# Kernel optimization log

Hardware: AMD Instinct MI355X
Metric: run time of the kernel (lower is better)

## Reference

```python
import jax, jax.numpy as jnp
import numpy as np


def setup_inputs() -> dict:
    key = jax.random.key(0)
    rain_hr = jax.random.normal(key, (16, 8, 1, 512, 512), dtype=jnp.float32)
    return {"rain_hr": rain_hr}


def reference(rain_hr):
    B, T, C, H, W = rain_hr.shape
    rain_mean = rain_hr.mean(axis=1)              # [B, C, H, W]

    fft = jnp.fft.fft2(rain_mean)                 # complex [B, C, H, W]
    power = jnp.abs(fft) ** 2                     # [B, C, H, W]

    # Integer radius map (torch: sqrt(...).long() truncates toward zero)
    ch, cw = H // 2, W // 2
    y = jnp.arange(H, dtype=jnp.float32) - ch
    x = jnp.arange(W, dtype=jnp.float32) - cw
    radius = jnp.sqrt(x[None, :] ** 2 + y[:, None] ** 2).astype(jnp.int32)  # [H, W]

    max_radius = min(H, W) // 2

    # power[..., mask].mean() == sum over (B, C, pixels at radius r) / (B*C*count_r)
    power_hw = power.sum(axis=(0, 1))             # [H, W]
    flat_r = radius.ravel()
    # out-of-range radii (>= max_radius) are dropped by segment_sum
    seg_sum = jax.ops.segment_sum(power_hw.ravel(), flat_r, num_segments=max_radius)
    counts = jax.ops.segment_sum(jnp.ones((H * W,), jnp.float32), flat_r, num_segments=max_radius)

    cnt = counts[1:]                               # radii 1 .. max_radius-1
    denom = jnp.maximum(cnt, 1.0) * (B * C)
    gen_spectrum = jnp.where(cnt > 0, seg_sum[1:] / denom, 0.0)

    k = jnp.arange(1, max_radius, dtype=jnp.float32)
    ref = k ** (-5.0 / 3.0)
    ref = ref / (ref.sum() + 1e-8)

    gen_norm = gen_spectrum / (gen_spectrum.sum() + 1e-8)
    loss = jnp.mean((gen_norm - ref) ** 2)
    return loss
```

## Files before the change

### kernel.cpp

```cpp
#include <hip/hip_runtime.h>
#include <math.h>

#define N 512
#define PLANE ((size_t)N * N)
#define NEG2PI (-6.28318530717958647692f)

__device__ inline void dft8(float (&xr)[8], float (&xi)[8]) {
    const float S = 0.70710678118654752440f;
    float t0r = xr[0] + xr[4], t0i = xi[0] + xi[4];
    float t4r = xr[0] - xr[4], t4i = xi[0] - xi[4];
    float t1r = xr[1] + xr[5], t1i = xi[1] + xi[5];
    float t5r = xr[1] - xr[5], t5i = xi[1] - xi[5];
    float t2r = xr[2] + xr[6], t2i = xi[2] + xi[6];
    float t6r = xr[2] - xr[6], t6i = xi[2] - xi[6];
    float t3r = xr[3] + xr[7], t3i = xi[3] + xi[7];
    float t7r = xr[3] - xr[7], t7i = xi[3] - xi[7];
    float o1r = S * (t5r + t5i), o1i = S * (t5i - t5r);
    float o2r = t6i,             o2i = -t6r;
    float o3r = S * (t7i - t7r), o3i = -S * (t7r + t7i);
    float p0r = t0r + t2r, p0i = t0i + t2i;
    float p1r = t1r + t3r, p1i = t1i + t3i;
    float q0r = t0r - t2r, q0i = t0i - t2i;
    float q1r = t1i - t3i, q1i = -(t1r - t3r);
    xr[0] = p0r + p1r; xi[0] = p0i + p1i;
    xr[4] = p0r - p1r; xi[4] = p0i - p1i;
    xr[2] = q0r + q1r; xi[2] = q0i + q1i;
    xr[6] = q0r - q1r; xi[6] = q0i - q1i;
    float r0r = t4r + o2r, r0i = t4i + o2i;
    float r1r = o1r + o3r, r1i = o1i + o3i;
    float u0r = t4r - o2r, u0i = t4i - o2i;
    float u1r = o1i - o3i, u1i = -(o1r - o3r);
    xr[1] = r0r + r1r; xi[1] = r0i + r1i;
    xr[5] = r0r - r1r; xi[5] = r0i - r1i;
    xr[3] = u0r + u1r; xi[3] = u0i + u1i;
    xr[7] = u0r - u1r; xi[7] = u0i - u1i;
}

__device__ inline void twiddle_apply(float (&xr)[8], float (&xi)[8], float ang1) {
    float ts, tc;
    __sincosf(ang1, &ts, &tc);
    float wr = tc, wi = ts;
    #pragma unroll
    for (int k = 1; k < 8; ++k) {
        float nr = xr[k] * wr - xi[k] * wi;
        float ni = xr[k] * wi + xi[k] * wr;
        xr[k] = nr; xi[k] = ni;
        float w2r = wr * tc - wi * ts;
        float w2i = wr * ts + wi * tc;
        wr = w2r; wi = w2i;
    }
}

__device__ inline void fft512_wave(float (&xr)[8], float (&xi)[8],
                                   float* sre, float* sim, const int l) {
    dft8(xr, xi);
    twiddle_apply(xr, xi, (NEG2PI / 512.0f) * (float)l);
    const int w0 = l + (l >> 3);
    #pragma unroll
    for (int k = 0; k < 8; ++k) { sre[72 * k + w0] = xr[k]; sim[72 * k + w0] = xi[k]; }
    const int i2 = l & 7;
    const int rbase = 72 * (l >> 3) + i2;
    #pragma unroll
    for (int q = 0; q < 8; ++q) { xr[q] = sre[rbase + 9 * q]; xi[q] = sim[rbase + 9 * q]; }
    dft8(xr, xi);
    twiddle_apply(xr, xi, (NEG2PI / 64.0f) * (float)i2);
    #pragma unroll
    for (int k = 0; k < 8; ++k) { sre[rbase + 9 * k] = xr[k]; sim[rbase + 9 * k] = xi[k]; }
    const int r3 = 9 * l;
    #pragma unroll
    for (int q = 0; q < 8; ++q) { xr[q] = sre[r3 + q]; xi[q] = sim[r3 + q]; }
    dft8(xr, xi);
}

__global__ __launch_bounds__(256, 4) void kern_rowfft(const float* __restrict__ in,
                                                      float2* __restrict__ ws) {
    __shared__ float sRe[4][576];
    __shared__ float sIm[4][576];
    const int wv = threadIdx.x >> 6;
    const int l  = threadIdx.x & 63;
    const int y  = blockIdx.x * 4 + wv;
    const int j  = blockIdx.y;
    const float* baseA = in + ((size_t)j * 8) * PLANE + (size_t)y * N;
    const float* baseB = in + ((size_t)(j + 8) * 8) * PLANE + (size_t)y * N;
    float* re = sRe[wv];
    float* im = sIm[wv];
    #pragma unroll
    for (int c0 = 0; c0 < 2; ++c0) {
        const int c = l + 64 * c0;
        float4 sa = make_float4(0.f, 0.f, 0.f, 0.f);
        float4 sb = make_float4(0.f, 0.f, 0.f, 0.f);
        #pragma unroll
        for (int tt = 0; tt < 8; ++tt) {
            float4 a = *(const float4*)(baseA + tt * PLANE + 4 * c);
            float4 b = *(const float4*)(baseB + tt * PLANE + 4 * c);
            sa.x += a.x; sa.y += a.y; sa.z += a.z; sa.w += a.w;
            sb.x += b.x; sb.y += b.y; sb.z += b.z; sb.w += b.w;
        }
        const int i0 = 4 * c;
        const int p0 = i0 + (i0 >> 3);
        re[p0 + 0] = sa.x * 0.125f; re[p0 + 1] = sa.y * 0.125f;
        re[p0 + 2] = sa.z * 0.125f; re[p0 + 3] = sa.w * 0.125f;
        im[p0 + 0] = sb.x * 0.125f; im[p0 + 1] = sb.y * 0.125f;
        im[p0 + 2] = sb.z * 0.125f; im[p0 + 3] = sb.w * 0.125f;
    }
    float xr[8], xi[8];
    #pragma unroll
    for (int q = 0; q < 8; ++q) {
        const int p = l + (l >> 3) + 72 * q;
        xr[q] = re[p]; xi[q] = im[p];
    }
    fft512_wave(xr, xi, re, im, l);
    float2* wp = ws + ((size_t)j << 18) + ((size_t)y << 9);
    #pragma unroll
    for (int k = 0; k < 8; ++k) {
        wp[64 * k + 8 * (l & 7) + (l >> 3)] = make_float2(xr[k], xi[k]);
    }
}

__global__ __launch_bounds__(512, 4) void kern_colfft(const float2* __restrict__ ws,
                                                      float* __restrict__ gseg,
                                                      float* __restrict__ gcnt) {
    __shared__ float sA[8 * 576];
    __shared__ float sB[8 * 576];
    __shared__ float lseg[256];
    __shared__ float lcnt[256];
    const int w   = threadIdx.x >> 6;
    const int l   = threadIdx.x & 63;
    const int fx0 = blockIdx.x * 8;
    const int j   = blockIdx.y;
    if (threadIdx.x < 256) { lseg[threadIdx.x] = 0.f; lcnt[threadIdx.x] = 0.f; }
    const float2* base = ws + ((size_t)j << 18) + fx0;
    #pragma unroll
    for (int i = 0; i < 8; ++i) {
        const int y = (w << 6) + (i << 3) + (l >> 3);
        const int f = l & 7;
        float2 v = base[((size_t)y << 9) + f];
        sA[y * 9 + f] = v.x;
        sB[y * 9 + f] = v.y;
    }
    __syncthreads();
    float xr[8], xi[8];
    #pragma unroll
    for (int q = 0; q < 8; ++q) {
        const int y = l + (q << 6);
        xr[q] = sA[y * 9 + w];
        xi[q] = sB[y * 9 + w];
    }
    __syncthreads();
    fft512_wave(xr, xi, sA + w * 576, sB + w * 576, l);
    const int dx  = fx0 + w - 256;
    const int dx2 = dx * dx;
    #pragma unroll
    for (int k = 0; k < 8; ++k) {
        const int fy = 64 * k + 8 * (l & 7) + (l >> 3);
        const int dy = fy - 256;
        const int d2 = dx2 + dy * dy;
        int r = (int)sqrtf((float)d2);
        if ((r + 1) * (r + 1) <= d2) r++;
        else if (r * r > d2) r--;
        if (r >= 1 && r < 256) {
            atomicAdd(&lseg[r], xr[k] * xr[k] + xi[k] * xi[k]);
            if (j == 0) atomicAdd(&lcnt[r], 1.0f);
        }
    }
    __syncthreads();
    const int t = threadIdx.x;
    if (t < 256) {
        if (lseg[t] != 0.f) atomicAdd(&gseg[j * 256 + t], lseg[t]);
    } else if (j == 0) {
        if (lcnt[t - 256] != 0.f) atomicAdd(&gcnt[t - 256], lcnt[t - 256]);
    }
}

__global__ __launch_bounds__(256) void kern_loss(const float* __restrict__ gseg,
                                                 const float* __restrict__ gcnt,
                                                 float* __restrict__ out) {
    __shared__ float red[256];
    const int t = threadIdx.x;
    float gen = 0.f, refv = 0.f;
    if (t >= 1) {
        float s = 0.f;
        #pragma unroll
        for (int j = 0; j < 8; ++j) s += gseg[j * 256 + t];
        float c = gcnt[t];
        gen  = (c > 0.f) ? s / (fmaxf(c, 1.f) * 16.0f) : 0.f;
        refv = powf((float)t, -5.0f / 3.0f);
    }
    red[t] = gen; __syncthreads();
    for (int off = 128; off > 0; off >>= 1) {
        if (t < off) red[t] += red[t + off];
        __syncthreads();
    }
    const float sgen = red[0]; __syncthreads();
    red[t] = refv; __syncthreads();
    for (int off = 128; off > 0; off >>= 1) {
        if (t < off) red[t] += red[t + off];
        __syncthreads();
    }
    const float sref = red[0]; __syncthreads();
    const float gn = gen  / (sgen + 1e-8f);
    const float rn = refv / (sref + 1e-8f);
    red[t] = (gn - rn) * (gn - rn); __syncthreads();
    for (int off = 128; off > 0; off >>= 1) {
        if (t < off) red[t] += red[t + off];
        __syncthreads();
    }
    if (t == 0) out[0] = red[0] / 255.0f;
}

extern "C" void kernel_launch(void* const* d_in, const int* in_sizes, int n_in,
                              void* d_out, int out_size, void* d_ws, size_t ws_size,
                              hipStream_t stream) {
    const float* in = (const float*)d_in[0];
    float2* planes = (float2*)d_ws;
    float* bins = (float*)((char*)d_ws + (size_t)8 * N * N * sizeof(float2));
    float* gseg = bins;
    float* gcnt = bins + 8 * 256;
    hipMemsetAsync(bins, 0, (8 * 256 + 256) * sizeof(float), stream);
    kern_rowfft<<<dim3(128, 8), 256, 0, stream>>>(in, planes);
    kern_colfft<<<dim3(64, 8), 512, 0, stream>>>(planes, gseg, gcnt);
    kern_loss<<<1, 256, 0, stream>>>(gseg, gcnt, (float*)d_out);
}
```

Before: 216.8 us.

## Fold memset and loss kernel into FFT kernels; shrink column-FFT blocks

Zeroing of the bins moves from a hipMemsetAsync into the row-FFT kernel, and the separate loss kernel is replaced by a last-block-done pattern inside the column FFT, using an atomic counter. The column FFT now runs four columns per 256-thread block, giving twice as many blocks, and loads them with float4 reads. This removes two launches and their gaps and raises block-level parallelism. In exchange it adds an atomic counter plus fences, and correctness now depends on the counter reset in the row kernel finishing before the column kernel starts.

Measured after the change: 252.0 us. 1.16x slower.

```diff
diff --git a/kernel.cpp b/kernel.cpp
--- a/kernel.cpp
+++ b/kernel.cpp
@@ -4,6 +4,7 @@
 #define N 512
 #define PLANE ((size_t)N * N)
 #define NEG2PI (-6.28318530717958647692f)
+#define NBLK_COL 1024
 
 __device__ inline void dft8(float (&xr)[8], float (&xi)[8]) {
     const float S = 0.70710678118654752440f;
@@ -73,13 +74,20 @@
 }
 
 __global__ __launch_bounds__(256, 4) void kern_rowfft(const float* __restrict__ in,
-                                                      float2* __restrict__ ws) {
+                                                      float2* __restrict__ ws,
+                                                      float* __restrict__ bins,
+                                                      unsigned int* __restrict__ done) {
     __shared__ float sRe[4][576];
     __shared__ float sIm[4][576];
     const int wv = threadIdx.x >> 6;
     const int l  = threadIdx.x & 63;
     const int y  = blockIdx.x * 4 + wv;
     const int j  = blockIdx.y;
+    if (blockIdx.x == 0 && j == 0) {
+        for (int i = threadIdx.x; i < 8 * 256 + 256; i += 256) bins[i] = 0.f;
+        if (threadIdx.x == 0)
+            __hip_atomic_store(done, 0u, __ATOMIC_RELAXED, __HIP_MEMORY_SCOPE_AGENT);
+    }
     const float* baseA = in + ((size_t)j * 8) * PLANE + (size_t)y * N;
     const float* baseB = in + ((size_t)(j + 8) * 8) * PLANE + (size_t)y * N;
     float* re = sRe[wv];
@@ -117,34 +125,40 @@
     }
 }
 
-__global__ __launch_bounds__(512, 4) void kern_colfft(const float2* __restrict__ ws,
+__global__ __launch_bounds__(256, 4) void kern_colfft(const float2* __restrict__ ws,
                                                       float* __restrict__ gseg,
-                                                      float* __restrict__ gcnt) {
-    __shared__ float sA[8 * 576];
-    __shared__ float sB[8 * 576];
+                                                      float* __restrict__ gcnt,
+                                                      unsigned int* __restrict__ done,
+                                                      float* __restrict__ out) {
+    __shared__ float sA[2560];
+    __shared__ float sB[2560];
     __shared__ float lseg[256];
     __shared__ float lcnt[256];
-    const int w   = threadIdx.x >> 6;
-    const int l   = threadIdx.x & 63;
-    const int fx0 = blockIdx.x * 8;
+    __shared__ int isLast;
+    const int t   = threadIdx.x;
+    const int w   = t >> 6;
+    const int l   = t & 63;
+    const int fx0 = blockIdx.x * 4;
     const int j   = blockIdx.y;
-    if (threadIdx.x < 256) { lseg[threadIdx.x] = 0.f; lcnt[threadIdx.x] = 0.f; }
+    lseg[t] = 0.f;
+    lcnt[t] = 0.f;
     const float2* base = ws + ((size_t)j << 18) + fx0;
     #pragma unroll
-    for (int i = 0; i < 8; ++i) {
-        const int y = (w << 6) + (i << 3) + (l >> 3);
-        const int f = l & 7;
-        float2 v = base[((size_t)y << 9) + f];
-        sA[y * 9 + f] = v.x;
-        sB[y * 9 + f] = v.y;
+    for (int i = 0; i < 4; ++i) {
+        const int g  = i * 256 + t;
+        const int y  = g >> 1;
+        const int fp = g & 1;
+        float4 v = *(const float4*)(base + ((size_t)y << 9) + 2 * fp);
+        sA[y * 5 + 2 * fp + 0] = v.x;  sB[y * 5 + 2 * fp + 0] = v.y;
+        sA[y * 5 + 2 * fp + 1] = v.z;  sB[y * 5 + 2 * fp + 1] = v.w;
     }
     __syncthreads();
     float xr[8], xi[8];
     #pragma unroll
     for (int q = 0; q < 8; ++q) {
         const int y = l + (q << 6);
-        xr[q] = sA[y * 9 + w];
-        xi[q] = sB[y * 9 + w];
+        xr[q] = sA[y * 5 + w];
+        xi[q] = sB[y * 5 + w];
     }
     __syncthreads();
     fft512_wave(xr, xi, sA + w * 576, sB + w * 576, l);
@@ -164,48 +178,50 @@
         }
     }
     __syncthreads();
-    const int t = threadIdx.x;
-    if (t < 256) {
-        if (lseg[t] != 0.f) atomicAdd(&gseg[j * 256 + t], lseg[t]);
-    } else if (j == 0) {
-        if (lcnt[t - 256] != 0.f) atomicAdd(&gcnt[t - 256], lcnt[t - 256]);
-    }
-}
-
-__global__ __launch_bounds__(256) void kern_loss(const float* __restrict__ gseg,
-                                                 const float* __restrict__ gcnt,
-                                                 float* __restrict__ out) {
-    __shared__ float red[256];
-    const int t = threadIdx.x;
+    if (lseg[t] != 0.f) atomicAdd(&gseg[j * 256 + t], lseg[t]);
+    if (j == 0 && lcnt[t] != 0.f) atomicAdd(&gcnt[t], lcnt[t]);
+    __syncthreads();
+    if (t == 0) {
+        __threadfence();
+        unsigned int old = __hip_atomic_fetch_add(done, 1u, __ATOMIC_ACQ_REL,
+                                                  __HIP_MEMORY_SCOPE_AGENT);
+        isLast = (old == NBLK_COL - 1) ? 1 : 0;
+    }
+    __syncthreads();
+    if (!isLast) return;
+    __threadfence();
     float gen = 0.f, refv = 0.f;
     if (t >= 1) {
         float s = 0.f;
         #pragma unroll
-        for (int j = 0; j < 8; ++j) s += gseg[j * 256 + t];
-        float c = gcnt[t];
+        for (int jj = 0; jj < 8; ++jj)
+            s += __hip_atomic_load(&gseg[jj * 256 + t], __ATOMIC_RELAXED,
+                                   __HIP_MEMORY_SCOPE_AGENT);
+        float c = __hip_atomic_load(&gcnt[t], __ATOMIC_RELAXED,
+                                    __HIP_MEMORY_SCOPE_AGENT);
         gen  = (c > 0.f) ? s / (fmaxf(c, 1.f) * 16.0f) : 0.f;
         refv = powf((float)t, -5.0f / 3.0f);
     }
-    red[t] = gen; __syncthreads();
+    lseg[t] = gen; __syncthreads();
     for (int off = 128; off > 0; off >>= 1) {
-        if (t < off) red[t] += red[t + off];
+        if (t < off) lseg[t] += lseg[t + off];
         __syncthreads();
     }
-    const float sgen = red[0]; __syncthreads();
-    red[t] = refv; __syncthreads();
+    const float sgen = lseg[0]; __syncthreads();
+    lseg[t] = refv; __syncthreads();
     for (int off = 128; off > 0; off >>= 1) {
-        if (t < off) red[t] += red[t + off];
+        if (t < off) lseg[t] += lseg[t + off];
         __syncthreads();
     }
-    const float sref = red[0]; __syncthreads();
+    const float sref = lseg[0]; __syncthreads();
     const float gn = gen  / (sgen + 1e-8f);
     const float rn = refv / (sref + 1e-8f);
-    red[t] = (gn - rn) * (gn - rn); __syncthreads();
+    lseg[t] = (gn - rn) * (gn - rn); __syncthreads();
     for (int off = 128; off > 0; off >>= 1) {
-        if (t < off) red[t] += red[t + off];
+        if (t < off) lseg[t] += lseg[t + off];
         __syncthreads();
     }
-    if (t == 0) out[0] = red[0] / 255.0f;
+    if (t == 0) out[0] = lseg[0] / 255.0f;
 }
 
 extern "C" void kernel_launch(void* const* d_in, const int* in_sizes, int n_in,
@@ -216,8 +232,8 @@
     float* bins = (float*)((char*)d_ws + (size_t)8 * N * N * sizeof(float2));
     float* gseg = bins;
     float* gcnt = bins + 8 * 256;
-    hipMemsetAsync(bins, 0, (8 * 256 + 256) * sizeof(float), stream);
-    kern_rowfft<<<dim3(128, 8), 256, 0, stream>>>(in, planes);
-    kern_colfft<<<dim3(64, 8), 512, 0, stream>>>(planes, gseg, gcnt);
-    kern_loss<<<1, 256, 0, stream>>>(gseg, gcnt, (float*)d_out);
-}
+    unsigned int* done = (unsigned int*)(bins + 8 * 256 + 256);
+    kern_rowfft<<<dim3(128, 8), 256, 0, stream>>>(in, planes, bins, done);
+    kern_colfft<<<dim3(128, 8), 256, 0, stream>>>(planes, gseg, gcnt, done,
+                                                  (float*)d_out);
+}
```
